# Kernel tuning notes

Hardware: AMD Instinct MI355X
Metric: run time of the kernel (lower is better)

## Reference

```python
import jax, jax.numpy as jnp
import numpy as np

N_POWER_ITER = 5


def _spectral_normalize(w, n_iter=N_POWER_ITER):
    # w: [out, in] 1x1-conv weight; divide by top singular value (power iteration,
    # deterministic init), mirroring torch.nn.utils.spectral_norm's reparameterization.
    u = jnp.full((w.shape[0],), 1.0 / np.sqrt(w.shape[0]), dtype=w.dtype)
    for _ in range(n_iter):
        v = w.T @ u
        v = v / (jnp.linalg.norm(v) + 1e-12)
        u = w @ v
        u = u / (jnp.linalg.norm(u) + 1e-12)
    sigma = u @ (w @ v)
    return w / sigma


def _maxpool2x2(x):
    # x: [B, C, H, W] -> [B, C, H//2, W//2]
    B, C, H, W = x.shape
    return x.reshape(B, C, H // 2, 2, W // 2, 2).max(axis=(3, 5))


def _conv1x1(w, x):
    # 1x1 conv == channel-mixing einsum. w: [out, in], x: [B, in, H, W]
    return jnp.einsum('oc,bchw->bohw', w, x)


def setup_inputs() -> dict:
    key = jax.random.key(0)
    kx, kq, kk, kv, ko = jax.random.split(key, 5)
    C = 512
    B, H, W = 16, 64, 64
    scale = 0.05
    return {
        'x': jax.random.normal(kx, (B, C, H, W), dtype=jnp.float32),
        'Wq': jax.random.normal(kq, (C // 8, C), dtype=jnp.float32) * scale,
        'Wk': jax.random.normal(kk, (C // 8, C), dtype=jnp.float32) * scale,
        'Wv': jax.random.normal(kv, (C // 2, C), dtype=jnp.float32) * scale,
        'Wo': jax.random.normal(ko, (C, C // 2), dtype=jnp.float32) * scale,
        'gamma': jnp.array([0.5], dtype=jnp.float32),
    }


def reference(x, Wq, Wk, Wv, Wo, gamma):
    B, C, H, W = x.shape
    n_ftrs = H * W
    wq = _spectral_normalize(Wq)
    wk = _spectral_normalize(Wk)
    wv = _spectral_normalize(Wv)
    wo = _spectral_normalize(Wo)
    f = _conv1x1(wq, x).reshape(B, C // 8, n_ftrs)                      # [B, C/8, HW]
    g = _maxpool2x2(_conv1x1(wk, x)).reshape(B, C // 8, n_ftrs // 4)    # [B, C/8, HW/4]
    h = _maxpool2x2(_conv1x1(wv, x)).reshape(B, C // 2, n_ftrs // 4)    # [B, C/2, HW/4]
    # scores: [B, HW, HW/4]; softmax over kv positions
    beta = jax.nn.softmax(jnp.einsum('bcn,bcm->bnm', f, g), axis=-1)
    # attention output: [B, C/2, HW]
    o = jnp.einsum('bcm,bnm->bcn', h, beta).reshape(B, C // 2, H, W)
    o = _conv1x1(wo, o)                                                 # [B, C, H, W]
    return gamma.reshape(()) * o + x
```

## Files before the change

kernel.cpp:

```cpp
#include <hip/hip_runtime.h>
#include <cstdint>

typedef __attribute__((ext_vector_type(8))) short bf16x8;
typedef __attribute__((ext_vector_type(4))) float f32x4;
typedef __attribute__((ext_vector_type(2))) unsigned int u32x2;

#define B_   16
#define C_   512
#define HW_  4096
#define M3_  384
#define HWP_ 1024
#define CV_  256

__device__ __forceinline__ unsigned short f2b(float f) {
  union { float f; unsigned u; } v; v.f = f;
  unsigned r = v.u + 0x7fffu + ((v.u >> 16) & 1u);
  return (unsigned short)(r >> 16);
}
__device__ __forceinline__ float b2f(unsigned short b) {
  union { unsigned u; float f; } v; v.u = ((unsigned)b) << 16;
  return v.f;
}
__device__ __forceinline__ f32x4 mfma16(bf16x8 a, bf16x8 b, f32x4 c) {
  return __builtin_amdgcn_mfma_f32_16x16x32_bf16(a, b, c, 0, 0, 0);
}
__device__ __forceinline__ void gload_lds16(const unsigned short* g, unsigned short* l) {
  __builtin_amdgcn_global_load_lds(
      (const __attribute__((address_space(1))) void*)g,
      (__attribute__((address_space(3))) void*)l, 16, 0, 0);
}

__global__ __launch_bounds__(256) void k_transpose(const float* __restrict__ x,
                                                   unsigned short* __restrict__ xb) {
  __shared__ unsigned short t[64][66];
  const int b = blockIdx.z, k0 = blockIdx.y * 64, n0 = blockIdx.x * 64;
  const float* xp = x + (size_t)b * C_ * HW_;
  const int ln = threadIdx.x & 63, g = threadIdx.x >> 6;
  for (int kk = g; kk < 64; kk += 4)
    t[kk][ln] = f2b(xp[(size_t)(k0 + kk) * HW_ + n0 + ln]);
  __syncthreads();
  unsigned short* xo = xb + (size_t)b * HW_ * C_;
  for (int nn = g; nn < 64; nn += 4)
    xo[(size_t)(n0 + nn) * C_ + k0 + ln] = t[ln][nn];
}

__global__ __launch_bounds__(256) void k_wtrans(
    const float* __restrict__ Wq, const float* __restrict__ Wk,
    const float* __restrict__ Wv, const float* __restrict__ Wo,
    float* __restrict__ wt) {
  const float* w; int out, in; float* dst;
  switch (blockIdx.z) {
    case 0: w = Wq; out = 64;  in = 512; dst = wt;          break;
    case 1: w = Wk; out = 64;  in = 512; dst = wt + 32768;  break;
    case 2: w = Wv; out = 256; in = 512; dst = wt + 65536;  break;
    default: w = Wo; out = 512; in = 256; dst = wt + 196608; break;
  }
  const int o0 = blockIdx.y * 64, i0 = blockIdx.x * 64;
  if (o0 >= out || i0 >= in) return;
  __shared__ float t[64][65];
  const int ln = threadIdx.x & 63, g = threadIdx.x >> 6;
  for (int oo = g; oo < 64; oo += 4)
    t[oo][ln] = w[(size_t)(o0 + oo) * in + i0 + ln];
  __syncthreads();
  for (int ii = g; ii < 64; ii += 4)
    dst[(size_t)(i0 + ii) * out + o0 + ln] = t[ln][ii];
}

__device__ __forceinline__ float breduce1024(float val, float* red) {
  __syncthreads();
#pragma unroll
  for (int off = 32; off > 0; off >>= 1) val += __shfl_down(val, off);
  if ((threadIdx.x & 63) == 0) red[threadIdx.x >> 6] = val;
  __syncthreads();
  float s = 0.f;
#pragma unroll
  for (int i = 0; i < 16; ++i) s += red[i];
  return s;
}

__global__ __launch_bounds__(1024) void k_specnorm(
    const float* __restrict__ Wq, const float* __restrict__ Wk,
    const float* __restrict__ Wv, const float* __restrict__ Wo,
    const float* __restrict__ wt,
    unsigned short* __restrict__ wqkv, unsigned short* __restrict__ wob) {
  __shared__ float u[512], v[512];
  __shared__ float part[4096];
  __shared__ float red[16];
  const float* w; const float* wT; int out, in; unsigned short* dst;
  switch (blockIdx.x) {
    case 0: w = Wq; wT = wt;          out = 64;  in = 512; dst = wqkv;             break;
    case 1: w = Wk; wT = wt + 32768;  out = 64;  in = 512; dst = wqkv + 64 * 512;  break;
    case 2: w = Wv; wT = wt + 65536;  out = 256; in = 512; dst = wqkv + 128 * 512; break;
    default: w = Wo; wT = wt + 196608; out = 512; in = 256; dst = wob;             break;
  }
  const int tid = threadIdx.x;
  const float rs = rsqrtf((float)out);
  if (tid < out) u[tid] = rs;
  __syncthreads();
  for (int it = 0; it < 5; ++it) {
    {
      const int G = in >> 2, nch = 1024 / G;
      const int ch = tid / G, grp = tid - ch * G;
      const int rpc = out / nch, obase = ch * rpc;
      f32x4 acc = {0.f, 0.f, 0.f, 0.f};
#pragma unroll 8
      for (int r = 0; r < rpc; ++r) {
        const int o = obase + r;
        const f32x4 wv = *reinterpret_cast<const f32x4*>(&w[(size_t)o * in + grp * 4]);
        const float uo = u[o];
        acc[0] += wv[0] * uo; acc[1] += wv[1] * uo;
        acc[2] += wv[2] * uo; acc[3] += wv[3] * uo;
      }
      *reinterpret_cast<f32x4*>(&part[ch * in + grp * 4]) = acc;
      __syncthreads();
      if (tid < in) {
        float s = 0.f;
        for (int c2 = 0; c2 < nch; ++c2) s += part[c2 * in + tid];
        v[tid] = s;
      }
    }
    {
      float ss = 0.f;
      __syncthreads();
      if (tid < in) ss = v[tid] * v[tid];
      ss = breduce1024(ss, red);
      const float sv = 1.f / (sqrtf(ss) + 1e-12f);
      if (tid < in) v[tid] *= sv;
      __syncthreads();
    }
    {
      const int G = out >> 2, nch = 1024 / G;
      const int ch = tid / G, grp = tid - ch * G;
      const int cpc = in / nch, cbase = ch * cpc;
      f32x4 acc = {0.f, 0.f, 0.f, 0.f};
#pragma unroll 8
      for (int r = 0; r < cpc; ++r) {
        const int c = cbase + r;
        const f32x4 wv = *reinterpret_cast<const f32x4*>(&wT[(size_t)c * out + grp * 4]);
        const float vc = v[c];
        acc[0] += wv[0] * vc; acc[1] += wv[1] * vc;
        acc[2] += wv[2] * vc; acc[3] += wv[3] * vc;
      }
      *reinterpret_cast<f32x4*>(&part[ch * out + grp * 4]) = acc;
      __syncthreads();
      if (tid < out) {
        float s = 0.f;
        for (int c2 = 0; c2 < nch; ++c2) s += part[c2 * out + tid];
        u[tid] = s;
      }
    }
    {
      float su = 0.f;
      __syncthreads();
      if (tid < out) su = u[tid] * u[tid];
      su = breduce1024(su, red);
      const float sv2 = 1.f / (sqrtf(su) + 1e-12f);
      if (tid < out) u[tid] *= sv2;
      __syncthreads();
    }
  }
  float sp = 0.f;
  {
    const int G = out >> 2, nch = 1024 / G;
    const int ch = tid / G, grp = tid - ch * G;
    const int cpc = in / nch, cbase = ch * cpc;
    f32x4 acc = {0.f, 0.f, 0.f, 0.f};
#pragma unroll 8
    for (int r = 0; r < cpc; ++r) {
      const int c = cbase + r;
      const f32x4 wv = *reinterpret_cast<const f32x4*>(&wT[(size_t)c * out + grp * 4]);
      const float vc = v[c];
      acc[0] += wv[0] * vc; acc[1] += wv[1] * vc;
      acc[2] += wv[2] * vc; acc[3] += wv[3] * vc;
    }
    *reinterpret_cast<f32x4*>(&part[ch * out + grp * 4]) = acc;
    __syncthreads();
    if (tid < out) {
      float s = 0.f;
      for (int c2 = 0; c2 < nch; ++c2) s += part[c2 * out + tid];
      sp = s * u[tid];
    }
  }
  sp = breduce1024(sp, red);
  const float oscale = (blockIdx.x == 0) ? 1.44269504f : 1.0f;
  const float inv_sigma = (1.f / sp) * oscale;
  const int total = out * in;
  for (int i = tid * 4; i < total; i += 4096) {
    const f32x4 wv = *reinterpret_cast<const f32x4*>(&w[i]);
    u32x2 pw;
    pw[0] = ((unsigned)f2b(wv[1] * inv_sigma) << 16) | f2b(wv[0] * inv_sigma);
    pw[1] = ((unsigned)f2b(wv[3] * inv_sigma) << 16) | f2b(wv[2] * inv_sigma);
    *reinterpret_cast<u32x2*>(&dst[i]) = pw;
  }
}

__global__ __launch_bounds__(256) void k_gemm_qkv(
    const unsigned short* __restrict__ xb, const unsigned short* __restrict__ wqkv,
    unsigned short* __restrict__ yt) {
  __shared__ alignas(16) char smem[32768];
  unsigned short* As = (unsigned short*)smem;
  unsigned short* Bs = (unsigned short*)(smem + 16384);
  const int lid = blockIdx.x;
  const int swz = (lid & 7) * 192 + (lid >> 3);
  const int mt = swz % 3, rest = swz / 3;
  const int nt = rest & 31, b = rest >> 5;
  const int n0 = nt * 128, m0 = mt * 128;
  const unsigned short* Ap = xb + (size_t)b * HW_ * C_ + (size_t)n0 * C_;
  const unsigned short* Bp = wqkv + (size_t)m0 * C_;
  const int tid = threadIdx.x, lane = tid & 63, wid = tid >> 6;
  const int wn = (wid >> 1) * 64, wm = (wid & 1) * 64;
  f32x4 acc[4][4] = {};
  for (int k0 = 0; k0 < C_; k0 += 64) {
    __syncthreads();
#pragma unroll
    for (int i = 0; i < 4; ++i) {
      const int r = i * 32 + (tid >> 3);
      const int s = tid & 7;
      const int rw = i * 32 + wid * 8;
      const size_t goff = (size_t)r * C_ + k0 + (size_t)((s ^ (r & 7)) * 8);
      gload_lds16(&Ap[goff], &As[rw * 64]);
      gload_lds16(&Bp[goff], &Bs[rw * 64]);
    }
    __syncthreads();
#pragma unroll
    for (int kk = 0; kk < 2; ++kk) {
      bf16x8 af[4], bfr[4];
#pragma unroll
      for (int i = 0; i < 4; ++i) {
        const int r = wn + i * 16 + (lane & 15);
        const int slot = (kk * 4 + (lane >> 4)) ^ (r & 7);
        af[i] = *reinterpret_cast<const bf16x8*>(&As[r * 64 + slot * 8]);
      }
#pragma unroll
      for (int j = 0; j < 4; ++j) {
        const int r = wm + j * 16 + (lane & 15);
        const int slot = (kk * 4 + (lane >> 4)) ^ (r & 7);
        bfr[j] = *reinterpret_cast<const bf16x8*>(&Bs[r * 64 + slot * 8]);
      }
#pragma unroll
      for (int i = 0; i < 4; ++i)
#pragma unroll
        for (int j = 0; j < 4; ++j) acc[i][j] = mfma16(af[i], bfr[j], acc[i][j]);
    }
  }
  unsigned short* eps = (unsigned short*)smem;
  unsigned short* Y = yt + (size_t)b * HW_ * M3_;
#pragma unroll
  for (int h = 0; h < 2; ++h) {
    __syncthreads();
    if ((wid >> 1) == h) {
#pragma unroll
      for (int i = 0; i < 4; ++i)
#pragma unroll
        for (int j = 0; j < 4; ++j)
#pragma unroll
          for (int r = 0; r < 4; ++r) {
            const int nl = i * 16 + (lane >> 4) * 4 + r;
            const int ml = wm + j * 16 + (lane & 15);
            eps[nl * 136 + ml] = f2b(acc[i][j][r]);
          }
    }
    __syncthreads();
#pragma unroll
    for (int t = 0; t < 4; ++t) {
      const int row = t * 16 + (tid >> 4);
      const int m8 = (tid & 15) * 8;
      *reinterpret_cast<f32x4*>(&Y[(size_t)(n0 + h * 64 + row) * M3_ + m0 + m8]) =
          *reinterpret_cast<const f32x4*>(&eps[row * 136 + m8]);
    }
  }
}

__global__ __launch_bounds__(256) void k_pool_g(const unsigned short* __restrict__ yt,
                                                unsigned short* __restrict__ gt) {
  const int b = blockIdx.y, mp0 = blockIdx.x * 64;
  const int c = threadIdx.x & 63, dm = threadIdx.x >> 6;
  const unsigned short* Y = yt + (size_t)b * HW_ * M3_;
  unsigned short* G = gt + (size_t)b * HWP_ * 64;
  for (int mm = dm; mm < 64; mm += 4) {
    const int mp = mp0 + mm;
    const int n00 = (mp >> 5) * 128 + (mp & 31) * 2;
    const float a0 = b2f(Y[(size_t)n00 * M3_ + 64 + c]);
    const float a1 = b2f(Y[(size_t)(n00 + 1) * M3_ + 64 + c]);
    const float a2 = b2f(Y[(size_t)(n00 + 64) * M3_ + 64 + c]);
    const float a3 = b2f(Y[(size_t)(n00 + 65) * M3_ + 64 + c]);
    G[(size_t)mp * 64 + c] = f2b(fmaxf(fmaxf(a0, a1), fmaxf(a2, a3)));
  }
}

__global__ __launch_bounds__(256) void k_pool_vt(const unsigned short* __restrict__ yt,
                                                 unsigned short* __restrict__ vt) {
  __shared__ unsigned short t[64][66];
  const int b = blockIdx.z, mp0 = blockIdx.x * 64, cv0 = blockIdx.y * 64;
  const unsigned short* Y = yt + (size_t)b * HW_ * M3_;
  const int c = threadIdx.x & 63, dm = threadIdx.x >> 6;
  for (int mm = dm; mm < 64; mm += 4) {
    const int mp = mp0 + mm;
    const int n00 = (mp >> 5) * 128 + (mp & 31) * 2;
    const float a0 = b2f(Y[(size_t)n00 * M3_ + 128 + cv0 + c]);
    const float a1 = b2f(Y[(size_t)(n00 + 1) * M3_ + 128 + cv0 + c]);
    const float a2 = b2f(Y[(size_t)(n00 + 64) * M3_ + 128 + cv0 + c]);
    const float a3 = b2f(Y[(size_t)(n00 + 65) * M3_ + 128 + cv0 + c]);
    t[mm][c] = f2b(fmaxf(fmaxf(a0, a1), fmaxf(a2, a3)));
  }
  __syncthreads();
  unsigned short* V = vt + (size_t)b * CV_ * HWP_;
  for (int cc = dm; cc < 64; cc += 4)
    V[(size_t)(cv0 + cc) * HWP_ + mp0 + c] = t[c][cc];
}

__global__ __launch_bounds__(256, 2) void k_attn(
    const unsigned short* __restrict__ yt, const unsigned short* __restrict__ gt,
    const unsigned short* __restrict__ vt, unsigned short* __restrict__ oat) {
  __shared__ alignas(16) char smem[59392];
  const int lid = blockIdx.x;
  const int swz = (lid & 7) * 64 + (lid >> 3);
  const int q0 = (swz & 31) * 128, b = swz >> 5;
  const int tid = threadIdx.x, lane = tid & 63, wid = tid >> 6;
  const int q = lane & 15, g = lane >> 4;
  const unsigned short* Qg = yt + (size_t)b * HW_ * M3_ + (size_t)(q0 + wid * 32) * M3_;
  const unsigned short* Gg = gt + (size_t)b * HWP_ * 64;
  const unsigned short* Vg = vt + (size_t)b * CV_ * HWP_;
  unsigned short* P = (unsigned short*)(smem + 49152) + wid * 1280;
  bf16x8 qf[2][2];
#pragma unroll
  for (int h = 0; h < 2; ++h)
#pragma unroll
    for (int kk = 0; kk < 2; ++kk)
      qf[h][kk] = *reinterpret_cast<const bf16x8*>(&Qg[(size_t)(h * 16 + q) * M3_ + kk * 32 + g * 8]);
  const int kr = tid >> 3, ks = tid & 7;
  f32x4 kreg, vreg[4];
  kreg = *reinterpret_cast<const f32x4*>(&Gg[(size_t)kr * 64 + ks * 8]);
#pragma unroll
  for (int t = 0; t < 4; ++t) {
    const int i = tid + t * 256, r = i >> 2, s = i & 3;
    vreg[t] = *reinterpret_cast<const f32x4*>(&Vg[(size_t)r * HWP_ + s * 8]);
  }
  {
    unsigned short* Kb = (unsigned short*)smem;
    unsigned short* Vb = (unsigned short*)(smem + 8192);
    *reinterpret_cast<f32x4*>(&Kb[kr * 64 + (ks ^ (kr & 7)) * 8]) = kreg;
#pragma unroll
    for (int t = 0; t < 4; ++t) {
      const int i = tid + t * 256, r = i >> 2, s = i & 3;
      *reinterpret_cast<f32x4*>(&Vb[r * 40 + s * 8]) = vreg[t];
    }
  }
  kreg = *reinterpret_cast<const f32x4*>(&Gg[(size_t)(32 + kr) * 64 + ks * 8]);
#pragma unroll
  for (int t = 0; t < 4; ++t) {
    const int i = tid + t * 256, r = i >> 2, s = i & 3;
    vreg[t] = *reinterpret_cast<const f32x4*>(&Vg[(size_t)r * HWP_ + 32 + s * 8]);
  }
  __syncthreads();
  f32x4 oacc[2][16] = {};
  float m_run[2] = {-1e30f, -1e30f}, l_run[2] = {0.f, 0.f};
  for (int it = 0; it < 32; ++it) {
    const int cur = it & 1;
    unsigned short* Kc = (unsigned short*)(smem + cur * 4096);
    unsigned short* Vc = (unsigned short*)(smem + 8192 + cur * 20480);
    if (it < 31) {
      unsigned short* Kn = (unsigned short*)(smem + (cur ^ 1) * 4096);
      unsigned short* Vn = (unsigned short*)(smem + 8192 + (cur ^ 1) * 20480);
      *reinterpret_cast<f32x4*>(&Kn[kr * 64 + (ks ^ (kr & 7)) * 8]) = kreg;
#pragma unroll
      for (int t = 0; t < 4; ++t) {
        const int i = tid + t * 256, r = i >> 2, s = i & 3;
        *reinterpret_cast<f32x4*>(&Vn[r * 40 + s * 8]) = vreg[t];
      }
    }
    if (it < 30) {
      const int kvn = (it + 2) * 32;
      kreg = *reinterpret_cast<const f32x4*>(&Gg[(size_t)(kvn + kr) * 64 + ks * 8]);
#pragma unroll
      for (int t = 0; t < 4; ++t) {
        const int i = tid + t * 256, r = i >> 2, s = i & 3;
        vreg[t] = *reinterpret_cast<const f32x4*>(&Vg[(size_t)r * HWP_ + kvn + s * 8]);
      }
    }
    f32x4 sacc[2][2] = {};
#pragma unroll
    for (int kk = 0; kk < 2; ++kk) {
      bf16x8 kf[2];
#pragma unroll
      for (int i = 0; i < 2; ++i) {
        const int row = i * 16 + q;
        const int sl = (kk * 4 + g) ^ (row & 7);
        kf[i] = *reinterpret_cast<const bf16x8*>(&Kc[row * 64 + sl * 8]);
      }
#pragma unroll
      for (int h = 0; h < 2; ++h)
#pragma unroll
        for (int i = 0; i < 2; ++i) sacc[h][i] = mfma16(kf[i], qf[h][kk], sacc[h][i]);
    }
#pragma unroll
    for (int h = 0; h < 2; ++h) {
      float tmax = -1e30f;
#pragma unroll
      for (int i = 0; i < 2; ++i)
#pragma unroll
        for (int r = 0; r < 4; ++r) tmax = fmaxf(tmax, sacc[h][i][r]);
      tmax = fmaxf(tmax, __shfl_xor(tmax, 16));
      tmax = fmaxf(tmax, __shfl_xor(tmax, 32));
      if (__any(tmax > m_run[h] + 11.0f)) {
        const float mnew = fmaxf(m_run[h], tmax);
        const float alpha = exp2f(m_run[h] - mnew);
        m_run[h] = mnew;
        l_run[h] *= alpha;
        float al[4];
#pragma unroll
        for (int r = 0; r < 4; ++r) al[r] = __shfl(alpha, g * 4 + r);
#pragma unroll
        for (int j = 0; j < 16; ++j) {
          oacc[h][j][0] *= al[0]; oacc[h][j][1] *= al[1];
          oacc[h][j][2] *= al[2]; oacc[h][j][3] *= al[3];
        }
      }
      const int qg = h * 16 + q;
      float lsum = 0.f;
#pragma unroll
      for (int i = 0; i < 2; ++i) {
        const float p0 = exp2f(sacc[h][i][0] - m_run[h]);
        const float p1 = exp2f(sacc[h][i][1] - m_run[h]);
        const float p2 = exp2f(sacc[h][i][2] - m_run[h]);
        const float p3 = exp2f(sacc[h][i][3] - m_run[h]);
        lsum += (p0 + p1) + (p2 + p3);
        u32x2 pw;
        pw[0] = ((unsigned)f2b(p1) << 16) | f2b(p0);
        pw[1] = ((unsigned)f2b(p3) << 16) | f2b(p2);
        const int c = 2 * i + (g >> 1);
        *reinterpret_cast<u32x2*>(&P[qg * 40 + c * 8 + (g & 1) * 4]) = pw;
      }
      lsum += __shfl_xor(lsum, 16);
      lsum += __shfl_xor(lsum, 32);
      l_run[h] += lsum;
    }
    __builtin_amdgcn_s_setprio(1);
    bf16x8 pa[2];
#pragma unroll
    for (int h = 0; h < 2; ++h) {
      const int qg = h * 16 + q;
      pa[h] = *reinterpret_cast<const bf16x8*>(&P[qg * 40 + g * 8]);
    }
#pragma unroll
    for (int j = 0; j < 16; ++j) {
      const int row = j * 16 + q;
      const bf16x8 vf = *reinterpret_cast<const bf16x8*>(&Vc[row * 40 + g * 8]);
      oacc[0][j] = mfma16(pa[0], vf, oacc[0][j]);
      oacc[1][j] = mfma16(pa[1], vf, oacc[1][j]);
    }
    __builtin_amdgcn_s_setprio(0);
    __syncthreads();
  }
  float linv[2][4];
#pragma unroll
  for (int h = 0; h < 2; ++h) {
    const float myinv = 1.f / l_run[h];
#pragma unroll
    for (int r = 0; r < 4; ++r) linv[h][r] = __shfl(myinv, g * 4 + r);
  }
  unsigned short* eps = (unsigned short*)smem;
  unsigned short* O = oat + (size_t)b * HW_ * CV_ + (size_t)q0 * CV_;
#pragma unroll
  for (int ch = 0; ch < 2; ++ch) {
    __syncthreads();
    if ((wid >> 1) == ch) {
#pragma unroll
      for (int h = 0; h < 2; ++h)
#pragma unroll
        for (int j = 0; j < 16; ++j)
#pragma unroll
          for (int r = 0; r < 4; ++r) {
            const int row = (wid & 1) * 32 + h * 16 + g * 4 + r;
            const int cv = j * 16 + q;
            eps[row * 264 + cv] = f2b(oacc[h][j][r] * linv[h][r]);
          }
    }
    __syncthreads();
#pragma unroll
    for (int t = 0; t < 8; ++t) {
      const int row = t * 8 + (tid >> 5);
      const int cv8 = (tid & 31) * 8;
      *reinterpret_cast<f32x4*>(&O[(size_t)(ch * 64 + row) * CV_ + cv8]) =
          *reinterpret_cast<const f32x4*>(&eps[row * 264 + cv8]);
    }
  }
}

__global__ __launch_bounds__(256) void k_gemm_out(
    const unsigned short* __restrict__ oat, const unsigned short* __restrict__ wob,
    const float* __restrict__ x, const float* __restrict__ gamma,
    float* __restrict__ out) {
  __shared__ alignas(16) char smem[32768];
  unsigned short* As = (unsigned short*)smem;
  unsigned short* Bs = (unsigned short*)(smem + 16384);
  const int lid = blockIdx.x;
  const int swz = (lid & 7) * 256 + (lid >> 3);
  const int ct = swz & 3, nt = (swz >> 2) & 31, b = swz >> 7;
  const int n0 = nt * 128, co0 = ct * 128;
  const unsigned short* Ap = wob + (size_t)co0 * CV_;
  const unsigned short* Bp = oat + (size_t)b * HW_ * CV_ + (size_t)n0 * CV_;
  const int tid = threadIdx.x, lane = tid & 63, wid = tid >> 6;
  const int wc = (wid >> 1) * 64, wn = (wid & 1) * 64;
  f32x4 acc[4][4] = {};
  for (int k0 = 0; k0 < CV_; k0 += 64) {
    __syncthreads();
#pragma unroll
    for (int i = 0; i < 4; ++i) {
      const int r = i * 32 + (tid >> 3);
      const int s = tid & 7;
      const int rw = i * 32 + wid * 8;
      const size_t goff = (size_t)r * CV_ + k0 + (size_t)((s ^ (r & 7)) * 8);
      gload_lds16(&Ap[goff], &As[rw * 64]);
      gload_lds16(&Bp[goff], &Bs[rw * 64]);
    }
    __syncthreads();
#pragma unroll
    for (int kk = 0; kk < 2; ++kk) {
      bf16x8 af[4], bfr[4];
#pragma unroll
      for (int i = 0; i < 4; ++i) {
        const int r = wc + i * 16 + (lane & 15);
        const int slot = (kk * 4 + (lane >> 4)) ^ (r & 7);
        af[i] = *reinterpret_cast<const bf16x8*>(&As[r * 64 + slot * 8]);
      }
#pragma unroll
      for (int j = 0; j < 4; ++j) {
        const int r = wn + j * 16 + (lane & 15);
        const int slot = (kk * 4 + (lane >> 4)) ^ (r & 7);
        bfr[j] = *reinterpret_cast<const bf16x8*>(&Bs[r * 64 + slot * 8]);
      }
#pragma unroll
      for (int i = 0; i < 4; ++i)
#pragma unroll
        for (int j = 0; j < 4; ++j) acc[i][j] = mfma16(af[i], bfr[j], acc[i][j]);
    }
  }
  float* eps = (float*)smem;
  const float g = gamma[0];
  const size_t base = (size_t)b * C_ * HW_;
#pragma unroll
  for (int h = 0; h < 4; ++h) {
    __syncthreads();
    if ((wid >> 1) == (h >> 1)) {
#pragma unroll
      for (int ii = 0; ii < 2; ++ii) {
        const int i = (h & 1) * 2 + ii;
#pragma unroll
        for (int j = 0; j < 4; ++j)
#pragma unroll
          for (int r = 0; r < 4; ++r) {
            const int col2 = ii * 16 + (lane >> 4) * 4 + r;
            const int nl = wn + j * 16 + (lane & 15);
            eps[col2 * 132 + nl] = acc[i][j][r];
          }
      }
    }
    __syncthreads();
#pragma unroll
    for (int t = 0; t < 4; ++t) {
      const int row = t * 8 + (tid >> 5);
      const int col = (tid & 31) * 4;
      const size_t goff = base + (size_t)(co0 + h * 32 + row) * HW_ + n0 + col;
      const f32x4 xv = *reinterpret_cast<const f32x4*>(&x[goff]);
      const f32x4 av = *reinterpret_cast<const f32x4*>(&eps[row * 132 + col]);
      f32x4 ov;
      ov[0] = g * av[0] + xv[0];
      ov[1] = g * av[1] + xv[1];
      ov[2] = g * av[2] + xv[2];
      ov[3] = g * av[3] + xv[3];
      *reinterpret_cast<f32x4*>(&out[goff]) = ov;
    }
  }
}

extern "C" void kernel_launch(void* const* d_in, const int* in_sizes, int n_in,
                              void* d_out, int out_size, void* d_ws, size_t ws_size,
                              hipStream_t stream) {
  (void)in_sizes; (void)n_in; (void)out_size; (void)ws_size;
  const float* x     = (const float*)d_in[0];
  const float* Wq    = (const float*)d_in[1];
  const float* Wk    = (const float*)d_in[2];
  const float* Wv    = (const float*)d_in[3];
  const float* Wo    = (const float*)d_in[4];
  const float* gamma = (const float*)d_in[5];
  float* out = (float*)d_out;
  char* ws = (char*)d_ws;

  unsigned short* wqkv = (unsigned short*)(ws);
  unsigned short* wob  = (unsigned short*)(ws + 393216);
  unsigned short* xb   = (unsigned short*)(ws + 655360);
  unsigned short* yt   = (unsigned short*)(ws + 67764224);
  unsigned short* gt   = (unsigned short*)(ws + 118095872);
  unsigned short* vt   = (unsigned short*)(ws + 120193024);
  unsigned short* oat  = xb;
  float* wt = (float*)yt;

  k_transpose<<<dim3(64, 8, 16), 256, 0, stream>>>(x, xb);
  k_wtrans<<<dim3(8, 8, 4), 256, 0, stream>>>(Wq, Wk, Wv, Wo, wt);
  k_specnorm<<<4, 1024, 0, stream>>>(Wq, Wk, Wv, Wo, wt, wqkv, wob);
  k_gemm_qkv<<<1536, 256, 0, stream>>>(xb, wqkv, yt);
  k_pool_g<<<dim3(16, 16), 256, 0, stream>>>(yt, gt);
  k_pool_vt<<<dim3(16, 4, 16), 256, 0, stream>>>(yt, vt);
  k_attn<<<512, 256, 0, stream>>>(yt, gt, vt, oat);
  k_gemm_out<<<2048, 256, 0, stream>>>(oat, wob, x, gamma, out);
}
```

Baseline: 292.2 us.

## Split attention block across 8 waves with 16 queries per wave

The attention kernel now launches 512 threads per block (8 waves), and each wave owns 16 query rows instead of 32. This halves the per-wave accumulator and score register state and spreads the K/V tile loads over more threads. The aim is more resident waves and better latency hiding. In exchange, each wave reads the K and V fragments from shared memory for only half as many queries, so LDS traffic per MFMA doubles, and block barriers now synchronise twice as many waves.

```diff
diff --git a/kernel.cpp b/kernel.cpp
--- a/kernel.cpp
+++ b/kernel.cpp
@@ -309,7 +309,7 @@
     V[(size_t)(cv0 + cc) * HWP_ + mp0 + c] = t[c][cc];
 }
 
-__global__ __launch_bounds__(256, 2) void k_attn(
+__global__ __launch_bounds__(512, 4) void k_attn(
     const unsigned short* __restrict__ yt, const unsigned short* __restrict__ gt,
     const unsigned short* __restrict__ vt, unsigned short* __restrict__ oat) {
   __shared__ alignas(16) char smem[59392];
@@ -318,43 +318,42 @@
   const int q0 = (swz & 31) * 128, b = swz >> 5;
   const int tid = threadIdx.x, lane = tid & 63, wid = tid >> 6;
   const int q = lane & 15, g = lane >> 4;
-  const unsigned short* Qg = yt + (size_t)b * HW_ * M3_ + (size_t)(q0 + wid * 32) * M3_;
+  const unsigned short* Qg = yt + (size_t)b * HW_ * M3_ + (size_t)(q0 + wid * 16) * M3_;
   const unsigned short* Gg = gt + (size_t)b * HWP_ * 64;
   const unsigned short* Vg = vt + (size_t)b * CV_ * HWP_;
-  unsigned short* P = (unsigned short*)(smem + 49152) + wid * 1280;
-  bf16x8 qf[2][2];
-#pragma unroll
-  for (int h = 0; h < 2; ++h)
-#pragma unroll
-    for (int kk = 0; kk < 2; ++kk)
-      qf[h][kk] = *reinterpret_cast<const bf16x8*>(&Qg[(size_t)(h * 16 + q) * M3_ + kk * 32 + g * 8]);
+  unsigned short* P = (unsigned short*)(smem + 49152) + wid * 640;
+  bf16x8 qf[2];
+#pragma unroll
+  for (int kk = 0; kk < 2; ++kk)
+    qf[kk] = *reinterpret_cast<const bf16x8*>(&Qg[(size_t)q * M3_ + kk * 32 + g * 8]);
   const int kr = tid >> 3, ks = tid & 7;
-  f32x4 kreg, vreg[4];
-  kreg = *reinterpret_cast<const f32x4*>(&Gg[(size_t)kr * 64 + ks * 8]);
-#pragma unroll
-  for (int t = 0; t < 4; ++t) {
-    const int i = tid + t * 256, r = i >> 2, s = i & 3;
+  f32x4 kreg, vreg[2];
+  if (tid < 256) kreg = *reinterpret_cast<const f32x4*>(&Gg[(size_t)kr * 64 + ks * 8]);
+#pragma unroll
+  for (int t = 0; t < 2; ++t) {
+    const int i = tid + t * 512, r = i >> 2, s = i & 3;
     vreg[t] = *reinterpret_cast<const f32x4*>(&Vg[(size_t)r * HWP_ + s * 8]);
   }
   {
     unsigned short* Kb = (unsigned short*)smem;
     unsigned short* Vb = (unsigned short*)(smem + 8192);
-    *reinterpret_cast<f32x4*>(&Kb[kr * 64 + (ks ^ (kr & 7)) * 8]) = kreg;
-#pragma unroll
-    for (int t = 0; t < 4; ++t) {
-      const int i = tid + t * 256, r = i >> 2, s = i & 3;
+    if (tid < 256)
+      *reinterpret_cast<f32x4*>(&Kb[kr * 64 + (ks ^ (kr & 7)) * 8]) = kreg;
+#pragma unroll
+    for (int t = 0; t < 2; ++t) {
+      const int i = tid + t * 512, r = i >> 2, s = i & 3;
       *reinterpret_cast<f32x4*>(&Vb[r * 40 + s * 8]) = vreg[t];
     }
   }
-  kreg = *reinterpret_cast<const f32x4*>(&Gg[(size_t)(32 + kr) * 64 + ks * 8]);
-#pragma unroll
-  for (int t = 0; t < 4; ++t) {
-    const int i = tid + t * 256, r = i >> 2, s = i & 3;
+  if (tid < 256) kreg = *reinterpret_cast<const f32x4*>(&Gg[(size_t)(32 + kr) * 64 + ks * 8]);
+#pragma unroll
+  for (int t = 0; t < 2; ++t) {
+    const int i = tid + t * 512, r = i >> 2, s = i & 3;
     vreg[t] = *reinterpret_cast<const f32x4*>(&Vg[(size_t)r * HWP_ + 32 + s * 8]);
   }
   __syncthreads();
-  f32x4 oacc[2][16] = {};
-  float m_run[2] = {-1e30f, -1e30f}, l_run[2] = {0.f, 0.f};
+  f32x4 oacc[16] = {};
+  float m_run = -1e30f, l_run = 0.f;
   for (int it = 0; it < 32; ++it) {
     const int cur = it & 1;
     unsigned short* Kc = (unsigned short*)(smem + cur * 4096);
@@ -362,23 +361,24 @@
     if (it < 31) {
       unsigned short* Kn = (unsigned short*)(smem + (cur ^ 1) * 4096);
       unsigned short* Vn = (unsigned short*)(smem + 8192 + (cur ^ 1) * 20480);
-      *reinterpret_cast<f32x4*>(&Kn[kr * 64 + (ks ^ (kr & 7)) * 8]) = kreg;
-#pragma unroll
-      for (int t = 0; t < 4; ++t) {
-        const int i = tid + t * 256, r = i >> 2, s = i & 3;
+      if (tid < 256)
+        *reinterpret_cast<f32x4*>(&Kn[kr * 64 + (ks ^ (kr & 7)) * 8]) = kreg;
+#pragma unroll
+      for (int t = 0; t < 2; ++t) {
+        const int i = tid + t * 512, r = i >> 2, s = i & 3;
         *reinterpret_cast<f32x4*>(&Vn[r * 40 + s * 8]) = vreg[t];
       }
     }
     if (it < 30) {
       const int kvn = (it + 2) * 32;
-      kreg = *reinterpret_cast<const f32x4*>(&Gg[(size_t)(kvn + kr) * 64 + ks * 8]);
-#pragma unroll
-      for (int t = 0; t < 4; ++t) {
-        const int i = tid + t * 256, r = i >> 2, s = i & 3;
+      if (tid < 256) kreg = *reinterpret_cast<const f32x4*>(&Gg[(size_t)(kvn + kr) * 64 + ks * 8]);
+#pragma unroll
+      for (int t = 0; t < 2; ++t) {
+        const int i = tid + t * 512, r = i >> 2, s = i & 3;
         vreg[t] = *reinterpret_cast<const f32x4*>(&Vg[(size_t)r * HWP_ + kvn + s * 8]);
       }
     }
-    f32x4 sacc[2][2] = {};
+    f32x4 sacc[2] = {};
 #pragma unroll
     for (int kk = 0; kk < 2; ++kk) {
       bf16x8 kf[2];
@@ -389,97 +389,81 @@
         kf[i] = *reinterpret_cast<const bf16x8*>(&Kc[row * 64 + sl * 8]);
       }
 #pragma unroll
-      for (int h = 0; h < 2; ++h)
-#pragma unroll
-        for (int i = 0; i < 2; ++i) sacc[h][i] = mfma16(kf[i], qf[h][kk], sacc[h][i]);
-    }
-#pragma unroll
-    for (int h = 0; h < 2; ++h) {
-      float tmax = -1e30f;
-#pragma unroll
-      for (int i = 0; i < 2; ++i)
-#pragma unroll
-        for (int r = 0; r < 4; ++r) tmax = fmaxf(tmax, sacc[h][i][r]);
-      tmax = fmaxf(tmax, __shfl_xor(tmax, 16));
-      tmax = fmaxf(tmax, __shfl_xor(tmax, 32));
-      if (__any(tmax > m_run[h] + 11.0f)) {
-        const float mnew = fmaxf(m_run[h], tmax);
-        const float alpha = exp2f(m_run[h] - mnew);
-        m_run[h] = mnew;
-        l_run[h] *= alpha;
-        float al[4];
-#pragma unroll
-        for (int r = 0; r < 4; ++r) al[r] = __shfl(alpha, g * 4 + r);
-#pragma unroll
-        for (int j = 0; j < 16; ++j) {
-          oacc[h][j][0] *= al[0]; oacc[h][j][1] *= al[1];
-          oacc[h][j][2] *= al[2]; oacc[h][j][3] *= al[3];
-        }
-      }
-      const int qg = h * 16 + q;
-      float lsum = 0.f;
-#pragma unroll
-      for (int i = 0; i < 2; ++i) {
-        const float p0 = exp2f(sacc[h][i][0] - m_run[h]);
-        const float p1 = exp2f(sacc[h][i][1] - m_run[h]);
-        const float p2 = exp2f(sacc[h][i][2] - m_run[h]);
-        const float p3 = exp2f(sacc[h][i][3] - m_run[h]);
-        lsum += (p0 + p1) + (p2 + p3);
-        u32x2 pw;
-        pw[0] = ((unsigned)f2b(p1) << 16) | f2b(p0);
-        pw[1] = ((unsigned)f2b(p3) << 16) | f2b(p2);
-        const int c = 2 * i + (g >> 1);
-        *reinterpret_cast<u32x2*>(&P[qg * 40 + c * 8 + (g & 1) * 4]) = pw;
-      }
-      lsum += __shfl_xor(lsum, 16);
-      lsum += __shfl_xor(lsum, 32);
-      l_run[h] += lsum;
-    }
+      for (int i = 0; i < 2; ++i) sacc[i] = mfma16(kf[i], qf[kk], sacc[i]);
+    }
+    float tmax = -1e30f;
+#pragma unroll
+    for (int i = 0; i < 2; ++i)
+#pragma unroll
+      for (int r = 0; r < 4; ++r) tmax = fmaxf(tmax, sacc[i][r]);
+    tmax = fmaxf(tmax, __shfl_xor(tmax, 16));
+    tmax = fmaxf(tmax, __shfl_xor(tmax, 32));
+    if (__any(tmax > m_run + 11.0f)) {
+      const float mnew = fmaxf(m_run, tmax);
+      const float alpha = exp2f(m_run - mnew);
+      m_run = mnew;
+      l_run *= alpha;
+      float al[4];
+#pragma unroll
+      for (int r = 0; r < 4; ++r) al[r] = __shfl(alpha, g * 4 + r);
+#pragma unroll
+      for (int j = 0; j < 16; ++j) {
+        oacc[j][0] *= al[0]; oacc[j][1] *= al[1];
+        oacc[j][2] *= al[2]; oacc[j][3] *= al[3];
+      }
+    }
+    float lsum = 0.f;
+#pragma unroll
+    for (int i = 0; i < 2; ++i) {
+      const float p0 = exp2f(sacc[i][0] - m_run);
+      const float p1 = exp2f(sacc[i][1] - m_run);
+      const float p2 = exp2f(sacc[i][2] - m_run);
+      const float p3 = exp2f(sacc[i][3] - m_run);
+      lsum += (p0 + p1) + (p2 + p3);
+      u32x2 pw;
+      pw[0] = ((unsigned)f2b(p1) << 16) | f2b(p0);
+      pw[1] = ((unsigned)f2b(p3) << 16) | f2b(p2);
+      *reinterpret_cast<u32x2*>(&P[q * 40 + i * 16 + g * 4]) = pw;
+    }
+    lsum += __shfl_xor(lsum, 16);
+    lsum += __shfl_xor(lsum, 32);
+    l_run += lsum;
     __builtin_amdgcn_s_setprio(1);
-    bf16x8 pa[2];
-#pragma unroll
-    for (int h = 0; h < 2; ++h) {
-      const int qg = h * 16 + q;
-      pa[h] = *reinterpret_cast<const bf16x8*>(&P[qg * 40 + g * 8]);
-    }
+    const bf16x8 pa = *reinterpret_cast<const bf16x8*>(&P[q * 40 + g * 8]);
 #pragma unroll
     for (int j = 0; j < 16; ++j) {
       const int row = j * 16 + q;
       const bf16x8 vf = *reinterpret_cast<const bf16x8*>(&Vc[row * 40 + g * 8]);
-      oacc[0][j] = mfma16(pa[0], vf, oacc[0][j]);
-      oacc[1][j] = mfma16(pa[1], vf, oacc[1][j]);
+      oacc[j] = mfma16(pa, vf, oacc[j]);
     }
     __builtin_amdgcn_s_setprio(0);
     __syncthreads();
   }
-  float linv[2][4];
-#pragma unroll
-  for (int h = 0; h < 2; ++h) {
-    const float myinv = 1.f / l_run[h];
-#pragma unroll
-    for (int r = 0; r < 4; ++r) linv[h][r] = __shfl(myinv, g * 4 + r);
+  float linv[4];
+  {
+    const float myinv = 1.f / l_run;
+#pragma unroll
+    for (int r = 0; r < 4; ++r) linv[r] = __shfl(myinv, g * 4 + r);
   }
   unsigned short* eps = (unsigned short*)smem;
   unsigned short* O = oat + (size_t)b * HW_ * CV_ + (size_t)q0 * CV_;
 #pragma unroll
   for (int ch = 0; ch < 2; ++ch) {
     __syncthreads();
-    if ((wid >> 1) == ch) {
-#pragma unroll
-      for (int h = 0; h < 2; ++h)
-#pragma unroll
-        for (int j = 0; j < 16; ++j)
-#pragma unroll
-          for (int r = 0; r < 4; ++r) {
-            const int row = (wid & 1) * 32 + h * 16 + g * 4 + r;
-            const int cv = j * 16 + q;
-            eps[row * 264 + cv] = f2b(oacc[h][j][r] * linv[h][r]);
-          }
-    }
-    __syncthreads();
-#pragma unroll
-    for (int t = 0; t < 8; ++t) {
-      const int row = t * 8 + (tid >> 5);
+    if ((wid >> 2) == ch) {
+#pragma unroll
+      for (int j = 0; j < 16; ++j)
+#pragma unroll
+        for (int r = 0; r < 4; ++r) {
+          const int row = (wid & 3) * 16 + g * 4 + r;
+          const int cv = j * 16 + q;
+          eps[row * 264 + cv] = f2b(oacc[j][r] * linv[r]);
+        }
+    }
+    __syncthreads();
+#pragma unroll
+    for (int t = 0; t < 4; ++t) {
+      const int row = t * 16 + (tid >> 5);
       const int cv8 = (tid & 31) * 8;
       *reinterpret_cast<f32x4*>(&O[(size_t)(ch * 64 + row) * CV_ + cv8]) =
           *reinterpret_cast<const f32x4*>(&eps[row * 264 + cv8]);
@@ -602,6 +586,6 @@
   k_gemm_qkv<<<1536, 256, 0, stream>>>(xb, wqkv, yt);
   k_pool_g<<<dim3(16, 16), 256, 0, stream>>>(yt, gt);
   k_pool_vt<<<dim3(16, 4, 16), 256, 0, stream>>>(yt, vt);
-  k_attn<<<512, 256, 0, stream>>>(yt, gt, vt, oat);
+  k_attn<<<512, 512, 0, stream>>>(yt, gt, vt, oat);
   k_gemm_out<<<2048, 256, 0, stream>>>(oat, wob, x, gamma, out);
 }
```

After: 296.7 us. About the same (+1.5%).
